# Kernel tuning notes

Hardware: AMD Instinct MI355X
Metric: run time of the kernel (lower is better)

The kernel has to match this reference:

```python
import jax, jax.numpy as jnp
import numpy as np

DECAY = 0.8      # cfg.ema_decay
EPS = 1e-5       # cfg.eps


def setup_inputs() -> dict:
    key = jax.random.key(0)
    k1, k2 = jax.random.split(key)
    H, B, N, D = 8, 8, 2048, 64   # num_codebooks, batch, seq, code_dim
    C = 1024                      # num_codes
    x = jax.random.normal(k1, (H, B, N, D), dtype=jnp.float32)
    embed = jax.random.normal(k2, (H, C, D), dtype=jnp.float32)
    embed_avg = embed.copy()
    cluster_size = jnp.ones((H, C), dtype=jnp.float32)
    return {"x": x, "embed": embed, "embed_avg": embed_avg, "cluster_size": cluster_size}


def reference(x, embed, embed_avg, cluster_size):
    # x: [h, b, n, d], embed: [h, c, d]
    h, b, n, d = x.shape
    c = embed.shape[1]
    flatten = x.reshape(h, b * n, d)  # pack 'h * d'

    # negative squared euclidean distance: -||f - e||^2
    f_sq = jnp.sum(flatten * flatten, axis=-1, keepdims=True)          # [h, N, 1]
    e_sq = jnp.sum(embed * embed, axis=-1)[:, None, :]                  # [h, 1, c]
    cross = jnp.einsum('hnd,hcd->hnc', flatten, embed)                  # [h, N, c]
    dist = -(f_sq - 2.0 * cross + e_sq)                                 # [h, N, c]

    # gumbel_sample with stochastic=False, straight_through=False -> argmax + one_hot
    embed_ind_flat = jnp.argmax(dist, axis=-1)                          # [h, N]
    embed_onehot = jax.nn.one_hot(embed_ind_flat, c, dtype=x.dtype)     # [h, N, c]

    # quantize (training path): onehot @ embed
    quantize = jnp.einsum('hnc,hcd->hnd', embed_onehot, embed).reshape(h, b, n, d)
    embed_ind = embed_ind_flat.reshape(h, b, n)

    # EMA codebook updates (ema_update=True, affine_params=False)
    cs_new = cluster_size * DECAY + embed_onehot.sum(axis=1) * (1.0 - DECAY)      # [h, c]
    embed_sum = jnp.einsum('hnd,hnc->hcd', flatten, embed_onehot)                  # [h, c, d]
    ea_new = embed_avg * DECAY + embed_sum * (1.0 - DECAY)                         # [h, c, d]

    ntot = jnp.sum(cs_new, axis=-1, keepdims=True)                                 # [h, 1]
    cs_smooth = (cs_new + EPS) / (ntot + c * EPS) * ntot                           # laplace smoothing * n
    embed_norm = ea_new / cs_smooth[..., None]                                     # new embed

    dist_out = dist.reshape(h, b, n, c)
    return quantize, embed_ind, embed_onehot, dist_out, embed_norm, ea_new, cs_new
```

## Files before the change

### kernel.cpp

```cpp
#include <hip/hip_runtime.h>

#define DECAY 0.8f
#define EPS   1e-5f
#define HN    8
#define BB    8
#define NSEQ  2048
#define DD    64
#define CC    1024
#define NROW  (BB*NSEQ)

#define TN 128
#define TC 128
#define PAD 4

__global__ void sumsq_kernel(const float* __restrict__ x, const float* __restrict__ embed,
                             float* __restrict__ fsq, float* __restrict__ esq) {
    int tid = blockIdx.x * blockDim.x + threadIdx.x;
    const int totalF = HN * NROW;
    const int totalE = HN * CC;
    if (tid < totalF) {
        const float4* src = (const float4*)(x + (size_t)tid * DD);
        float s = 0.f;
        #pragma unroll
        for (int i = 0; i < DD/4; ++i) {
            float4 v = src[i];
            s = fmaf(v.x, v.x, s); s = fmaf(v.y, v.y, s);
            s = fmaf(v.z, v.z, s); s = fmaf(v.w, v.w, s);
        }
        fsq[tid] = s;
    } else if (tid < totalF + totalE) {
        int t = tid - totalF;
        const float4* src = (const float4*)(embed + (size_t)t * DD);
        float s = 0.f;
        #pragma unroll
        for (int i = 0; i < DD/4; ++i) {
            float4 v = src[i];
            s = fmaf(v.x, v.x, s); s = fmaf(v.y, v.y, s);
            s = fmaf(v.z, v.z, s); s = fmaf(v.w, v.w, s);
        }
        esq[t] = s;
    }
}

__global__ __launch_bounds__(256)
void dist_argmax_kernel(const float* __restrict__ x, const float* __restrict__ embed,
                        const float* __restrict__ fsq, const float* __restrict__ esq,
                        float* __restrict__ out_q, float* __restrict__ out_i,
                        float* __restrict__ out_oh, float* __restrict__ out_d) {
    __shared__ float xs[DD][TN + PAD];
    __shared__ float es[DD][TC + PAD];

    const int h   = blockIdx.y;
    const int n0  = blockIdx.x * TN;
    const int tid = threadIdx.x;

    const float* xh = x     + (size_t)h * NROW * DD;
    const float* eh = embed + (size_t)h * CC   * DD;

    {
        int f4 = tid & 15;
        int r0 = tid >> 4;
        #pragma unroll
        for (int it = 0; it < TN/16; ++it) {
            int r = r0 + it*16;
            float4 v = *(const float4*)(xh + (size_t)(n0 + r)*DD + f4*4);
            int d = f4*4;
            xs[d+0][r] = v.x; xs[d+1][r] = v.y; xs[d+2][r] = v.z; xs[d+3][r] = v.w;
        }
    }

    const int ty = tid >> 4;
    const int tx = tid & 15;

    float fs[8];
    #pragma unroll
    for (int i = 0; i < 8; ++i) fs[i] = fsq[h*NROW + n0 + ty*8 + i];

    float bestv[8];
    int   besti[8];
    #pragma unroll
    for (int i = 0; i < 8; ++i) { bestv[i] = -3.4e38f; besti[i] = 0; }

    for (int c0 = 0; c0 < CC; c0 += TC) {
        __syncthreads();
        {
            int f4 = tid & 15;
            int r0 = tid >> 4;
            #pragma unroll
            for (int it = 0; it < TC/16; ++it) {
                int cc = r0 + it*16;
                float4 v = *(const float4*)(eh + (size_t)(c0 + cc)*DD + f4*4);
                int d = f4*4;
                es[d+0][cc] = v.x; es[d+1][cc] = v.y; es[d+2][cc] = v.z; es[d+3][cc] = v.w;
            }
        }
        __syncthreads();

        float acc[8][8];
        #pragma unroll
        for (int i = 0; i < 8; ++i)
            #pragma unroll
            for (int j = 0; j < 8; ++j) acc[i][j] = 0.f;

        #pragma unroll 4
        for (int k = 0; k < DD; ++k) {
            float a[8], b[8];
            *(float4*)&a[0] = *(const float4*)&xs[k][ty*8];
            *(float4*)&a[4] = *(const float4*)&xs[k][ty*8 + 4];
            *(float4*)&b[0] = *(const float4*)&es[k][tx*8];
            *(float4*)&b[4] = *(const float4*)&es[k][tx*8 + 4];
            #pragma unroll
            for (int i = 0; i < 8; ++i)
                #pragma unroll
                for (int j = 0; j < 8; ++j)
                    acc[i][j] = fmaf(a[i], b[j], acc[i][j]);
        }

        float eq[8];
        *(float4*)&eq[0] = *(const float4*)(esq + h*CC + c0 + tx*8);
        *(float4*)&eq[4] = *(const float4*)(esq + h*CC + c0 + tx*8 + 4);

        #pragma unroll
        for (int i = 0; i < 8; ++i) {
            int row = n0 + ty*8 + i;
            float dv[8];
            #pragma unroll
            for (int j = 0; j < 8; ++j)
                dv[j] = fmaf(2.f, acc[i][j], -(fs[i] + eq[j]));

            size_t ob = ((size_t)h*NROW + row)*CC + c0 + tx*8;
            *(float4*)(out_d + ob)     = make_float4(dv[0], dv[1], dv[2], dv[3]);
            *(float4*)(out_d + ob + 4) = make_float4(dv[4], dv[5], dv[6], dv[7]);
            float4 z = make_float4(0.f, 0.f, 0.f, 0.f);
            *(float4*)(out_oh + ob)     = z;
            *(float4*)(out_oh + ob + 4) = z;

            #pragma unroll
            for (int j = 0; j < 8; ++j) {
                if (dv[j] > bestv[i]) { bestv[i] = dv[j]; besti[i] = c0 + tx*8 + j; }
            }
        }
    }

    __syncthreads();

    #pragma unroll
    for (int i = 0; i < 8; ++i) {
        float v  = bestv[i];
        int   id = besti[i];
        #pragma unroll
        for (int off = 8; off >= 1; off >>= 1) {
            float ov = __shfl_xor(v, off, 64);
            int   oi = __shfl_xor(id, off, 64);
            if (ov > v || (ov == v && oi < id)) { v = ov; id = oi; }
        }
        int row = n0 + ty*8 + i;
        float4 qv = *(const float4*)(eh + (size_t)id*DD + tx*4);
        *(float4*)(out_q + ((size_t)h*NROW + row)*DD + tx*4) = qv;
        if (tx == 0) {
            out_i[(size_t)h*NROW + row] = (float)id;
            out_oh[((size_t)h*NROW + row)*CC + id] = 1.0f;
        }
    }
}

__global__ __launch_bounds__(64)
void ema_kernel(const float* __restrict__ x, const float* __restrict__ embed_avg,
                const float* __restrict__ cluster_size, const float* __restrict__ ind_f,
                float* __restrict__ out_cs, float* __restrict__ out_ea,
                float* __restrict__ out_norm) {
    const int h    = blockIdx.y;
    const int c    = blockIdx.x;
    const int lane = threadIdx.x;

    const float* cs_h = cluster_size + h*CC;
    float s = 0.f;
    #pragma unroll
    for (int i = 0; i < CC/64; ++i) s += cs_h[lane + i*64];
    #pragma unroll
    for (int off = 32; off >= 1; off >>= 1) s += __shfl_xor(s, off, 64);

    const float* xh   = x     + (size_t)h * NROW * DD;
    const float* indh = ind_f + (size_t)h * NROW;

    float sum_d = 0.f;
    int   cnt   = 0;
    for (int chunk = 0; chunk < NROW/64; ++chunk) {
        int myidx = (int)indh[chunk*64 + lane];
        unsigned long long m = __ballot(myidx == c);
        while (m) {
            int t = __ffsll(m) - 1;
            m &= m - 1;
            int n = chunk*64 + t;
            sum_d += xh[(size_t)n*DD + lane];
            cnt++;
        }
    }

    float csn  = cs_h[c]*DECAY + (float)cnt*(1.f - DECAY);
    float ea   = embed_avg[((size_t)h*CC + c)*DD + lane]*DECAY + sum_d*(1.f - DECAY);
    float ntot = s*DECAY + (1.f - DECAY)*(float)NROW;
    float css  = (csn + EPS) / (ntot + (float)CC*EPS) * ntot;

    out_ea  [((size_t)h*CC + c)*DD + lane] = ea;
    out_norm[((size_t)h*CC + c)*DD + lane] = ea / css;
    if (lane == 0) out_cs[h*CC + c] = csn;
}

extern "C" void kernel_launch(void* const* d_in, const int* in_sizes, int n_in,
                              void* d_out, int out_size, void* d_ws, size_t ws_size,
                              hipStream_t stream) {
    const float* x            = (const float*)d_in[0];
    const float* embed        = (const float*)d_in[1];
    const float* embed_avg    = (const float*)d_in[2];
    const float* cluster_size = (const float*)d_in[3];

    float* out = (float*)d_out;
    float* fsq = (float*)d_ws;
    float* esq = fsq + (size_t)HN * NROW;

    float* out_q    = out;
    float* out_i    = out_q    + (size_t)HN * NROW * DD;
    float* out_oh   = out_i    + (size_t)HN * NROW;
    float* out_d    = out_oh   + (size_t)HN * NROW * CC;
    float* out_norm = out_d    + (size_t)HN * NROW * CC;
    float* out_ea   = out_norm + (size_t)HN * CC * DD;
    float* out_cs   = out_ea   + (size_t)HN * CC * DD;

    {
        int total = HN*NROW + HN*CC;
        sumsq_kernel<<<(total + 255)/256, 256, 0, stream>>>(x, embed, fsq, esq);
    }
    {
        dim3 g(NROW/TN, HN);
        dist_argmax_kernel<<<g, 256, 0, stream>>>(x, embed, fsq, esq,
                                                  out_q, out_i, out_oh, out_d);
    }
    {
        dim3 g(CC, HN);
        ema_kernel<<<g, 64, 0, stream>>>(x, embed_avg, cluster_size, out_i,
                                         out_cs, out_ea, out_norm);
    }
}
```

Measured before the change: 585.3 us.

## Prefetch next codebook tile into registers and vectorize shared-memory transposes

The distance kernel now loads the next 128-code embed tile into registers while computing the current tile, then writes it to shared memory between barriers, overlapping global latency with FMA work. Shared-memory staging uses a 4x4 in-register transpose so stores are float4 instead of scalar, padding is removed, and each thread's column assignment is split into two 64-apart groups to cut bank conflicts on reads. It also sets launch bounds for two blocks per CU. Costs are more register pressure and dependence on hand-placed waitcnt and barriers for correctness.

```diff
diff --git a/kernel.cpp b/kernel.cpp
--- a/kernel.cpp
+++ b/kernel.cpp
@@ -9,9 +9,9 @@
 #define CC    1024
 #define NROW  (BB*NSEQ)
 
-#define TN 128
-#define TC 128
-#define PAD 4
+#define LS 128
+#define XS(k,r) xs[(k)*LS + (r)]
+#define ES(k,c) es[(k)*LS + (c)]
 
 __global__ void sumsq_kernel(const float* __restrict__ x, const float* __restrict__ embed,
                              float* __restrict__ fsq, float* __restrict__ esq) {
@@ -42,35 +42,59 @@
     }
 }
 
-__global__ __launch_bounds__(256)
-void dist_argmax_kernel(const float* __restrict__ x, const float* __restrict__ embed,
-                        const float* __restrict__ fsq, const float* __restrict__ esq,
-                        float* __restrict__ out_q, float* __restrict__ out_i,
-                        float* __restrict__ out_oh, float* __restrict__ out_d) {
-    __shared__ float xs[DD][TN + PAD];
-    __shared__ float es[DD][TC + PAD];
+__global__ __launch_bounds__(256, 2)
+void dist_fp32_kernel(const float* __restrict__ x, const float* __restrict__ embed,
+                      const float* __restrict__ fsq, const float* __restrict__ esq,
+                      float* __restrict__ out_q, float* __restrict__ out_i,
+                      float* __restrict__ out_oh, float* __restrict__ out_d) {
+    __shared__ float xs[64 * LS];
+    __shared__ float es[64 * LS];
 
     const int h   = blockIdx.y;
-    const int n0  = blockIdx.x * TN;
+    const int n0  = blockIdx.x * 128;
     const int tid = threadIdx.x;
-
-    const float* xh = x     + (size_t)h * NROW * DD;
-    const float* eh = embed + (size_t)h * CC   * DD;
-
-    {
-        int f4 = tid & 15;
-        int r0 = tid >> 4;
-        #pragma unroll
-        for (int it = 0; it < TN/16; ++it) {
-            int r = r0 + it*16;
-            float4 v = *(const float4*)(xh + (size_t)(n0 + r)*DD + f4*4);
-            int d = f4*4;
-            xs[d+0][r] = v.x; xs[d+1][r] = v.y; xs[d+2][r] = v.z; xs[d+3][r] = v.w;
-        }
-    }
-
-    const int ty = tid >> 4;
-    const int tx = tid & 15;
+    const int ty  = tid >> 4;
+    const int tx  = tid & 15;
+
+    const float* xh_   = x     + (size_t)h * NROW * DD;
+    const float* eh_   = embed + (size_t)h * CC   * DD;
+    const float* esq_h = esq   + h * CC;
+
+    const int g4 = (tid & 31) * 4;
+    const int k0 = (tid >> 5) * 8;
+
+    {
+        float4 v[2][4];
+        #pragma unroll
+        for (int t = 0; t < 2; ++t)
+            #pragma unroll
+            for (int i = 0; i < 4; ++i)
+                v[t][i] = *(const float4*)(xh_ + (size_t)(n0 + g4 + i) * DD + k0 + t*4);
+        #pragma unroll
+        for (int t = 0; t < 2; ++t) {
+            *(float4*)&XS(k0+t*4+0, g4) = make_float4(v[t][0].x, v[t][1].x, v[t][2].x, v[t][3].x);
+            *(float4*)&XS(k0+t*4+1, g4) = make_float4(v[t][0].y, v[t][1].y, v[t][2].y, v[t][3].y);
+            *(float4*)&XS(k0+t*4+2, g4) = make_float4(v[t][0].z, v[t][1].z, v[t][2].z, v[t][3].z);
+            *(float4*)&XS(k0+t*4+3, g4) = make_float4(v[t][0].w, v[t][1].w, v[t][2].w, v[t][3].w);
+        }
+    }
+    {
+        float4 v[2][4];
+        #pragma unroll
+        for (int t = 0; t < 2; ++t)
+            #pragma unroll
+            for (int i = 0; i < 4; ++i)
+                v[t][i] = *(const float4*)(eh_ + (size_t)(g4 + i) * DD + k0 + t*4);
+        #pragma unroll
+        for (int t = 0; t < 2; ++t) {
+            *(float4*)&ES(k0+t*4+0, g4) = make_float4(v[t][0].x, v[t][1].x, v[t][2].x, v[t][3].x);
+            *(float4*)&ES(k0+t*4+1, g4) = make_float4(v[t][0].y, v[t][1].y, v[t][2].y, v[t][3].y);
+            *(float4*)&ES(k0+t*4+2, g4) = make_float4(v[t][0].z, v[t][1].z, v[t][2].z, v[t][3].z);
+            *(float4*)&ES(k0+t*4+3, g4) = make_float4(v[t][0].w, v[t][1].w, v[t][2].w, v[t][3].w);
+        }
+    }
+    asm volatile("s_waitcnt lgkmcnt(0)" ::: "memory");
+    __builtin_amdgcn_s_barrier();
 
     float fs[8];
     #pragma unroll
@@ -81,20 +105,18 @@
     #pragma unroll
     for (int i = 0; i < 8; ++i) { bestv[i] = -3.4e38f; besti[i] = 0; }
 
-    for (int c0 = 0; c0 < CC; c0 += TC) {
-        __syncthreads();
-        {
-            int f4 = tid & 15;
-            int r0 = tid >> 4;
-            #pragma unroll
-            for (int it = 0; it < TC/16; ++it) {
-                int cc = r0 + it*16;
-                float4 v = *(const float4*)(eh + (size_t)(c0 + cc)*DD + f4*4);
-                int d = f4*4;
-                es[d+0][cc] = v.x; es[d+1][cc] = v.y; es[d+2][cc] = v.z; es[d+3][cc] = v.w;
-            }
-        }
-        __syncthreads();
+    #pragma unroll 1
+    for (int ci = 0; ci < 8; ++ci) {
+        const int c0 = ci * 128;
+
+        float4 ev[2][4];
+        if (ci < 7) {
+            #pragma unroll
+            for (int t = 0; t < 2; ++t)
+                #pragma unroll
+                for (int i = 0; i < 4; ++i)
+                    ev[t][i] = *(const float4*)(eh_ + (size_t)(c0 + 128 + g4 + i) * DD + k0 + t*4);
+        }
 
         float acc[8][8];
         #pragma unroll
@@ -103,12 +125,12 @@
             for (int j = 0; j < 8; ++j) acc[i][j] = 0.f;
 
         #pragma unroll 4
-        for (int k = 0; k < DD; ++k) {
+        for (int k = 0; k < 64; ++k) {
             float a[8], b[8];
-            *(float4*)&a[0] = *(const float4*)&xs[k][ty*8];
-            *(float4*)&a[4] = *(const float4*)&xs[k][ty*8 + 4];
-            *(float4*)&b[0] = *(const float4*)&es[k][tx*8];
-            *(float4*)&b[4] = *(const float4*)&es[k][tx*8 + 4];
+            *(float4*)&a[0] = *(const float4*)&XS(k, ty*8);
+            *(float4*)&a[4] = *(const float4*)&XS(k, ty*8 + 4);
+            *(float4*)&b[0] = *(const float4*)&ES(k, tx*4);
+            *(float4*)&b[4] = *(const float4*)&ES(k, 64 + tx*4);
             #pragma unroll
             for (int i = 0; i < 8; ++i)
                 #pragma unroll
@@ -117,8 +139,8 @@
         }
 
         float eq[8];
-        *(float4*)&eq[0] = *(const float4*)(esq + h*CC + c0 + tx*8);
-        *(float4*)&eq[4] = *(const float4*)(esq + h*CC + c0 + tx*8 + 4);
+        *(float4*)&eq[0] = *(const float4*)(esq_h + c0 + tx*4);
+        *(float4*)&eq[4] = *(const float4*)(esq_h + c0 + 64 + tx*4);
 
         #pragma unroll
         for (int i = 0; i < 8; ++i) {
@@ -128,21 +150,39 @@
             for (int j = 0; j < 8; ++j)
                 dv[j] = fmaf(2.f, acc[i][j], -(fs[i] + eq[j]));
 
-            size_t ob = ((size_t)h*NROW + row)*CC + c0 + tx*8;
-            *(float4*)(out_d + ob)     = make_float4(dv[0], dv[1], dv[2], dv[3]);
-            *(float4*)(out_d + ob + 4) = make_float4(dv[4], dv[5], dv[6], dv[7]);
+            size_t rb = ((size_t)h*NROW + row)*CC + c0;
+            *(float4*)(out_d + rb + tx*4)       = make_float4(dv[0], dv[1], dv[2], dv[3]);
+            *(float4*)(out_d + rb + 64 + tx*4)  = make_float4(dv[4], dv[5], dv[6], dv[7]);
             float4 z = make_float4(0.f, 0.f, 0.f, 0.f);
-            *(float4*)(out_oh + ob)     = z;
-            *(float4*)(out_oh + ob + 4) = z;
-
-            #pragma unroll
-            for (int j = 0; j < 8; ++j) {
-                if (dv[j] > bestv[i]) { bestv[i] = dv[j]; besti[i] = c0 + tx*8 + j; }
+            *(float4*)(out_oh + rb + tx*4)      = z;
+            *(float4*)(out_oh + rb + 64 + tx*4) = z;
+
+            #pragma unroll
+            for (int j = 0; j < 4; ++j) {
+                if (dv[j] > bestv[i]) { bestv[i] = dv[j]; besti[i] = c0 + tx*4 + j; }
             }
-        }
-    }
-
-    __syncthreads();
+            #pragma unroll
+            for (int j = 4; j < 8; ++j) {
+                if (dv[j] > bestv[i]) { bestv[i] = dv[j]; besti[i] = c0 + 64 + tx*4 + (j-4); }
+            }
+        }
+
+        if (ci < 7) {
+            asm volatile("s_waitcnt lgkmcnt(0)" ::: "memory");
+            __builtin_amdgcn_s_barrier();
+            #pragma unroll
+            for (int t = 0; t < 2; ++t) {
+                *(float4*)&ES(k0+t*4+0, g4) = make_float4(ev[t][0].x, ev[t][1].x, ev[t][2].x, ev[t][3].x);
+                *(float4*)&ES(k0+t*4+1, g4) = make_float4(ev[t][0].y, ev[t][1].y, ev[t][2].y, ev[t][3].y);
+                *(float4*)&ES(k0+t*4+2, g4) = make_float4(ev[t][0].z, ev[t][1].z, ev[t][2].z, ev[t][3].z);
+                *(float4*)&ES(k0+t*4+3, g4) = make_float4(ev[t][0].w, ev[t][1].w, ev[t][2].w, ev[t][3].w);
+            }
+            asm volatile("s_waitcnt lgkmcnt(0)" ::: "memory");
+            __builtin_amdgcn_s_barrier();
+        }
+    }
+
+    asm volatile("s_waitcnt vmcnt(0)" ::: "memory");
 
     #pragma unroll
     for (int i = 0; i < 8; ++i) {
@@ -155,7 +195,7 @@
             if (ov > v || (ov == v && oi < id)) { v = ov; id = oi; }
         }
         int row = n0 + ty*8 + i;
-        float4 qv = *(const float4*)(eh + (size_t)id*DD + tx*4);
+        float4 qv = *(const float4*)(eh_ + (size_t)id*DD + tx*4);
         *(float4*)(out_q + ((size_t)h*NROW + row)*DD + tx*4) = qv;
         if (tx == 0) {
             out_i[(size_t)h*NROW + row] = (float)id;
@@ -232,9 +272,9 @@
         sumsq_kernel<<<(total + 255)/256, 256, 0, stream>>>(x, embed, fsq, esq);
     }
     {
-        dim3 g(NROW/TN, HN);
-        dist_argmax_kernel<<<g, 256, 0, stream>>>(x, embed, fsq, esq,
-                                                  out_q, out_i, out_oh, out_d);
+        dim3 g(NROW/128, HN);
+        dist_fp32_kernel<<<g, 256, 0, stream>>>(x, embed, fsq, esq,
+                                                out_q, out_i, out_oh, out_d);
     }
     {
         dim3 g(CC, HN);
```

After: 579.6 us. Within noise of the previous version (-1.0%).

## Pre-transpose codebook, read it from global, use nontemporal stores and 512-thread blocks

Applied to the files above, without the earlier changes.

Adds a transpose kernel that writes the codebook as [h, d, c] to workspace. The distance kernel then loads embedding columns straight from global/L2 instead of staging them through shared memory each code tile, which removes the per-tile barriers. It also moves to 512 threads with a 4x8 per-thread tile and writes the huge dist and one-hot outputs with nontemporal stores. The trade-off is more global/L2 load traffic per FMA and an extra small kernel launch.

```diff
diff --git a/kernel.cpp b/kernel.cpp
--- a/kernel.cpp
+++ b/kernel.cpp
@@ -9,9 +9,9 @@
 #define CC    1024
 #define NROW  (BB*NSEQ)
 
-#define TN 128
-#define TC 128
-#define PAD 4
+#define XS(k,r) xs[(k)*128 + (r)]
+
+typedef float vf4 __attribute__((ext_vector_type(4)));
 
 __global__ void sumsq_kernel(const float* __restrict__ x, const float* __restrict__ embed,
                              float* __restrict__ fsq, float* __restrict__ esq) {
@@ -43,97 +43,117 @@
 }
 
 __global__ __launch_bounds__(256)
-void dist_argmax_kernel(const float* __restrict__ x, const float* __restrict__ embed,
-                        const float* __restrict__ fsq, const float* __restrict__ esq,
-                        float* __restrict__ out_q, float* __restrict__ out_i,
-                        float* __restrict__ out_oh, float* __restrict__ out_d) {
-    __shared__ float xs[DD][TN + PAD];
-    __shared__ float es[DD][TC + PAD];
+void transpose_kernel(const float* __restrict__ e, float* __restrict__ eT) {
+    __shared__ float t[64][68];
+    const int h  = blockIdx.y;
+    const int c0 = blockIdx.x * 64;
+    const float* eh  = e  + (size_t)h * CC * DD;
+    float*       eTh = eT + (size_t)h * DD * CC;
+    const int r = threadIdx.x >> 4;
+    const int q = threadIdx.x & 15;
+
+    #pragma unroll
+    for (int rr = 0; rr < 4; ++rr) {
+        int cl = rr*16 + r;
+        float4 v = *(const float4*)(eh + (size_t)(c0 + cl)*DD + q*4);
+        t[q*4+0][cl] = v.x; t[q*4+1][cl] = v.y; t[q*4+2][cl] = v.z; t[q*4+3][cl] = v.w;
+    }
+    __syncthreads();
+    #pragma unroll
+    for (int rr = 0; rr < 4; ++rr) {
+        int k = rr*16 + r;
+        float4 w = *(const float4*)&t[k][q*4];
+        *(float4*)(eTh + (size_t)k*CC + c0 + q*4) = w;
+    }
+}
+
+__global__ __launch_bounds__(512, 4)
+void dist_fp32_kernel(const float* __restrict__ x, const float* __restrict__ embed,
+                      const float* __restrict__ eT,
+                      const float* __restrict__ fsq, const float* __restrict__ esq,
+                      float* __restrict__ out_q, float* __restrict__ out_i,
+                      float* __restrict__ out_oh, float* __restrict__ out_d) {
+    __shared__ float xs[64 * 128];
 
     const int h   = blockIdx.y;
-    const int n0  = blockIdx.x * TN;
+    const int n0  = blockIdx.x * 128;
     const int tid = threadIdx.x;
-
-    const float* xh = x     + (size_t)h * NROW * DD;
-    const float* eh = embed + (size_t)h * CC   * DD;
-
-    {
-        int f4 = tid & 15;
-        int r0 = tid >> 4;
-        #pragma unroll
-        for (int it = 0; it < TN/16; ++it) {
-            int r = r0 + it*16;
-            float4 v = *(const float4*)(xh + (size_t)(n0 + r)*DD + f4*4);
-            int d = f4*4;
-            xs[d+0][r] = v.x; xs[d+1][r] = v.y; xs[d+2][r] = v.z; xs[d+3][r] = v.w;
-        }
-    }
-
-    const int ty = tid >> 4;
-    const int tx = tid & 15;
-
-    float fs[8];
-    #pragma unroll
-    for (int i = 0; i < 8; ++i) fs[i] = fsq[h*NROW + n0 + ty*8 + i];
-
-    float bestv[8];
-    int   besti[8];
-    #pragma unroll
-    for (int i = 0; i < 8; ++i) { bestv[i] = -3.4e38f; besti[i] = 0; }
-
-    for (int c0 = 0; c0 < CC; c0 += TC) {
-        __syncthreads();
-        {
-            int f4 = tid & 15;
-            int r0 = tid >> 4;
-            #pragma unroll
-            for (int it = 0; it < TC/16; ++it) {
-                int cc = r0 + it*16;
-                float4 v = *(const float4*)(eh + (size_t)(c0 + cc)*DD + f4*4);
-                int d = f4*4;
-                es[d+0][cc] = v.x; es[d+1][cc] = v.y; es[d+2][cc] = v.z; es[d+3][cc] = v.w;
-            }
-        }
-        __syncthreads();
-
-        float acc[8][8];
-        #pragma unroll
-        for (int i = 0; i < 8; ++i)
+    const int ty  = tid >> 4;
+    const int tx  = tid & 15;
+
+    const float* xh_   = x     + (size_t)h * NROW * DD;
+    const float* eh_   = embed + (size_t)h * CC   * DD;
+    const float* eT_h  = eT    + (size_t)h * DD   * CC;
+    const float* esq_h = esq   + h * CC;
+
+    {
+        const int g4 = (tid & 31) * 4;
+        const int k0 = (tid >> 5) * 4;
+        float4 v[4];
+        #pragma unroll
+        for (int i = 0; i < 4; ++i)
+            v[i] = *(const float4*)(xh_ + (size_t)(n0 + g4 + i) * DD + k0);
+        *(float4*)&XS(k0+0, g4) = make_float4(v[0].x, v[1].x, v[2].x, v[3].x);
+        *(float4*)&XS(k0+1, g4) = make_float4(v[0].y, v[1].y, v[2].y, v[3].y);
+        *(float4*)&XS(k0+2, g4) = make_float4(v[0].z, v[1].z, v[2].z, v[3].z);
+        *(float4*)&XS(k0+3, g4) = make_float4(v[0].w, v[1].w, v[2].w, v[3].w);
+    }
+    asm volatile("s_waitcnt lgkmcnt(0)" ::: "memory");
+    __builtin_amdgcn_s_barrier();
+
+    float fs[4];
+    #pragma unroll
+    for (int i = 0; i < 4; ++i) fs[i] = fsq[h*NROW + n0 + ty*4 + i];
+
+    float bestv[4];
+    int   besti[4];
+    #pragma unroll
+    for (int i = 0; i < 4; ++i) { bestv[i] = -3.4e38f; besti[i] = 0; }
+
+    #pragma unroll 1
+    for (int ci = 0; ci < 8; ++ci) {
+        const int c0 = ci * 128;
+        const float* bbase = eT_h + c0 + tx*8;
+
+        float acc[4][8];
+        #pragma unroll
+        for (int i = 0; i < 4; ++i)
             #pragma unroll
             for (int j = 0; j < 8; ++j) acc[i][j] = 0.f;
 
         #pragma unroll 4
-        for (int k = 0; k < DD; ++k) {
-            float a[8], b[8];
-            *(float4*)&a[0] = *(const float4*)&xs[k][ty*8];
-            *(float4*)&a[4] = *(const float4*)&xs[k][ty*8 + 4];
-            *(float4*)&b[0] = *(const float4*)&es[k][tx*8];
-            *(float4*)&b[4] = *(const float4*)&es[k][tx*8 + 4];
-            #pragma unroll
-            for (int i = 0; i < 8; ++i)
+        for (int k = 0; k < 64; ++k) {
+            float a[4], b[8];
+            *(float4*)&a[0] = *(const float4*)&XS(k, ty*4);
+            *(float4*)&b[0] = *(const float4*)(bbase + (size_t)k*CC);
+            *(float4*)&b[4] = *(const float4*)(bbase + (size_t)k*CC + 4);
+            #pragma unroll
+            for (int i = 0; i < 4; ++i)
                 #pragma unroll
                 for (int j = 0; j < 8; ++j)
                     acc[i][j] = fmaf(a[i], b[j], acc[i][j]);
         }
 
         float eq[8];
-        *(float4*)&eq[0] = *(const float4*)(esq + h*CC + c0 + tx*8);
-        *(float4*)&eq[4] = *(const float4*)(esq + h*CC + c0 + tx*8 + 4);
-
-        #pragma unroll
-        for (int i = 0; i < 8; ++i) {
-            int row = n0 + ty*8 + i;
+        *(float4*)&eq[0] = *(const float4*)(esq_h + c0 + tx*8);
+        *(float4*)&eq[4] = *(const float4*)(esq_h + c0 + tx*8 + 4);
+
+        const vf4 z = {0.f, 0.f, 0.f, 0.f};
+        #pragma unroll
+        for (int i = 0; i < 4; ++i) {
+            int row = n0 + ty*4 + i;
             float dv[8];
             #pragma unroll
             for (int j = 0; j < 8; ++j)
                 dv[j] = fmaf(2.f, acc[i][j], -(fs[i] + eq[j]));
 
-            size_t ob = ((size_t)h*NROW + row)*CC + c0 + tx*8;
-            *(float4*)(out_d + ob)     = make_float4(dv[0], dv[1], dv[2], dv[3]);
-            *(float4*)(out_d + ob + 4) = make_float4(dv[4], dv[5], dv[6], dv[7]);
-            float4 z = make_float4(0.f, 0.f, 0.f, 0.f);
-            *(float4*)(out_oh + ob)     = z;
-            *(float4*)(out_oh + ob + 4) = z;
+            size_t rb = ((size_t)h*NROW + row)*CC + c0 + tx*8;
+            vf4 d0 = {dv[0], dv[1], dv[2], dv[3]};
+            vf4 d1 = {dv[4], dv[5], dv[6], dv[7]};
+            __builtin_nontemporal_store(d0, (vf4*)(out_d + rb));
+            __builtin_nontemporal_store(d1, (vf4*)(out_d + rb + 4));
+            __builtin_nontemporal_store(z,  (vf4*)(out_oh + rb));
+            __builtin_nontemporal_store(z,  (vf4*)(out_oh + rb + 4));
 
             #pragma unroll
             for (int j = 0; j < 8; ++j) {
@@ -142,10 +162,10 @@
         }
     }
 
-    __syncthreads();
-
-    #pragma unroll
-    for (int i = 0; i < 8; ++i) {
+    asm volatile("s_waitcnt vmcnt(0)" ::: "memory");
+
+    #pragma unroll
+    for (int i = 0; i < 4; ++i) {
         float v  = bestv[i];
         int   id = besti[i];
         #pragma unroll
@@ -154,8 +174,8 @@
             int   oi = __shfl_xor(id, off, 64);
             if (ov > v || (ov == v && oi < id)) { v = ov; id = oi; }
         }
-        int row = n0 + ty*8 + i;
-        float4 qv = *(const float4*)(eh + (size_t)id*DD + tx*4);
+        int row = n0 + ty*4 + i;
+        float4 qv = *(const float4*)(eh_ + (size_t)id*DD + tx*4);
         *(float4*)(out_q + ((size_t)h*NROW + row)*DD + tx*4) = qv;
         if (tx == 0) {
             out_i[(size_t)h*NROW + row] = (float)id;
@@ -218,6 +238,7 @@
     float* out = (float*)d_out;
     float* fsq = (float*)d_ws;
     float* esq = fsq + (size_t)HN * NROW;
+    float* eT  = esq + (size_t)HN * CC;
 
     float* out_q    = out;
     float* out_i    = out_q    + (size_t)HN * NROW * DD;
@@ -232,9 +253,13 @@
         sumsq_kernel<<<(total + 255)/256, 256, 0, stream>>>(x, embed, fsq, esq);
     }
     {
-        dim3 g(NROW/TN, HN);
-        dist_argmax_kernel<<<g, 256, 0, stream>>>(x, embed, fsq, esq,
-                                                  out_q, out_i, out_oh, out_d);
+        dim3 g(CC/64, HN);
+        transpose_kernel<<<g, 256, 0, stream>>>(embed, eT);
+    }
+    {
+        dim3 g(NROW/128, HN);
+        dist_fp32_kernel<<<g, 512, 0, stream>>>(x, embed, eT, fsq, esq,
+                                                out_q, out_i, out_oh, out_d);
     }
     {
         dim3 g(CC, HN);
```

New measurement: 633.3 us. 8.2% more time.
